# Kernel tuning notes

Hardware: AMD Instinct MI355X
Metric: run time of the kernel (lower is better)

The kernel has to match this reference:

```python
import jax, jax.numpy as jnp
import numpy as np

NUM_RBF = 16
TOP_K = 30
MAXREL = 32  # max_relative_feature
M_CTX = 16   # ligand context atoms per residue

PT_GROUP = jnp.array([0,1,18,1,2,13,14,15,16,17,18,1,2,13,14,15,16,17,18,1,2,3,4,5,6,7,8,9,10,11,12,13,14,15,16,17,18,1,2,3,4,5,6,7,8,9,10,11,12,13,14,15,16,17,18,1,2,3,3,3,3,3,3,3,3,3,3,3,3,3,3,3,4,5,6,7,8,9,10,11,12,13,14,15,16,17,18,1,2,3,3,3,3,3,3,3,3,3,3,3,3,3,3,3,4,5,6,7,8,9,10,11,12,13,14,15,16,17,18], dtype=jnp.int32)
PT_PERIOD = jnp.array([0,1,1,2,2,2,2,2,2,2,2,3,3,3,3,3,3,3,3,4,4,4,4,4,4,4,4,4,4,4,4,4,4,4,4,4,4,5,5,5,5,5,5,5,5,5,5,5,5,5,5,5,5,5,5,6,6,6,6,6,6,6,6,6,6,6,6,6,6,6,6,6,6,6,6,6,6,6,6,6,6,6,6,6,6,6,6,7,7,7,7,7,7,7,7,7,7,7,7,7,7,7,7,7,7,7,7,7,7,7,7,7,7,7,7,7,7,7,7], dtype=jnp.int32)

# pair order after the Ca-Ca term: (N,N),(C,C),(O,O),(Cb,Cb),(Ca,N),(Ca,C),(Ca,O),(Ca,Cb),
# (N,C),(N,O),(N,Cb),(Cb,C),(Cb,O),(O,C),(N,Ca),(C,Ca),(O,Ca),(Cb,Ca),(C,N),(O,N),(Cb,N),(C,Cb),(O,Cb),(C,O)
# atom index in A5 stack: N=0, Ca=1, C=2, O=3, Cb=4
AI = np.array([0,2,3,4,1,1,1,1,0,0,0,4,4,3,0,2,3,4,2,3,4,2,3,2])
BI = np.array([0,2,3,4,0,2,3,4,2,3,4,2,3,2,1,1,1,1,0,0,0,4,4,3])


def _rbf(D):
    mu = jnp.linspace(2.0, 22.0, NUM_RBF)
    sigma = (22.0 - 2.0) / NUM_RBF
    return jnp.exp(-(((D[..., None] - mu) / sigma) ** 2))


def _angle_features(A, Bc, Cc, Y):
    v1 = A - Bc
    v2 = Cc - Bc
    e1 = v1 / jnp.linalg.norm(v1, axis=-1, keepdims=True)
    dot = jnp.einsum('bli,bli->bl', e1, v2)[..., None]
    u2 = v2 - e1 * dot
    e2 = u2 / jnp.linalg.norm(u2, axis=-1, keepdims=True)
    e3 = jnp.cross(e1, e2, axis=-1)
    R = jnp.concatenate((e1[..., None], e2[..., None], e3[..., None]), axis=-1)  # [B,L,3,3]
    lv = jnp.einsum('blqp,blyq->blyp', R, Y - Bc[:, :, None, :])
    rxy = jnp.sqrt(lv[..., 0] ** 2 + lv[..., 1] ** 2 + 1e-8)
    f1 = lv[..., 0] / rxy
    f2 = lv[..., 1] / rxy
    rxyz = jnp.linalg.norm(lv, axis=-1) + 1e-8
    f3 = rxy / rxyz
    f4 = lv[..., 2] / rxyz
    return jnp.stack([f1, f2, f3, f4], axis=-1)  # [B,L,M,4]


def setup_inputs() -> dict:
    key = jax.random.key(0)
    ks = jax.random.split(key, 16)
    B, L, M = 2, 2048, M_CTX
    X = jax.random.normal(ks[0], (B, L, 4, 3), jnp.float32) * 10.0
    Y = jax.random.normal(ks[1], (B, L, M, 3), jnp.float32) * 10.0
    mask = jnp.ones((B, L), jnp.float32)
    Y_m = jnp.ones((B, L, M), jnp.float32)
    R_idx = jnp.arange(B * L, dtype=jnp.int32).reshape(B, L)
    chain_labels = jax.random.randint(ks[2], (B, L), 0, 2, jnp.int32)
    Y_t = jax.random.randint(ks[3], (B, L, M), 1, 119, jnp.int32)
    def lin(k, fi, fo):
        return jax.random.normal(k, (fi, fo), jnp.float32) / np.sqrt(fi)
    params = dict(
        Wp=lin(ks[4], 2 * MAXREL + 2, 16), bp=jnp.zeros((16,), jnp.float32),
        We=lin(ks[5], 16 + 25 * NUM_RBF, 128), be=jnp.zeros((128,), jnp.float32),
        Wn=lin(ks[6], 5 * NUM_RBF + 64 + 4, 128), bn=jnp.zeros((128,), jnp.float32),
        Wt=lin(ks[7], 147, 64), bt=jnp.zeros((64,), jnp.float32),
        Wyn=lin(ks[8], 147, 128), byn=jnp.zeros((128,), jnp.float32),
        Wye=lin(ks[9], NUM_RBF, 128), bye=jnp.zeros((128,), jnp.float32),
    )
    return dict(X=X, Y=Y, mask=mask, Y_m=Y_m, R_idx=R_idx, chain_labels=chain_labels, Y_t=Y_t, **params)


def reference(X, Y, mask, Y_m, R_idx, chain_labels, Y_t,
              Wp, bp, We, be, Wn, bn, Wt, bt, Wyn, byn, Wye, bye):
    B, L = X.shape[0], X.shape[1]
    N, Ca, C, O = X[:, :, 0], X[:, :, 1], X[:, :, 2], X[:, :, 3]
    b_ = Ca - N
    c_ = C - Ca
    a_ = jnp.cross(b_, c_, axis=-1)
    Cb = -0.58273431 * a_ + 0.56802827 * b_ - 0.54067466 * c_ + Ca

    # masked pairwise distances + kNN (smallest-k)
    m2 = mask[:, None, :] * mask[:, :, None]
    dX = Ca[:, None, :, :] - Ca[:, :, None, :]
    D = m2 * jnp.sqrt(jnp.sum(dX * dX, -1) + 1e-6)
    Dadj = D + (1.0 - m2) * jnp.max(D, -1, keepdims=True)
    k = min(TOP_K, L)
    negD, E_idx = jax.lax.top_k(-Dadj, k)
    D_neighbors = -negD  # [B,L,K]

    # gather all 5 atom coords of neighbors once, then all 24 cross-atom RBFs
    A5 = jnp.stack([N, Ca, C, O, Cb], axis=2)  # [B,L,5,3]
    nb = A5[jnp.arange(B)[:, None, None], E_idx]  # [B,L,K,5,3]
    dvec = A5[:, :, None, AI, :] - nb[:, :, :, BI, :]  # [B,L,K,24,3]
    Dp = jnp.sqrt(jnp.sum(dvec * dvec, -1) + 1e-6)
    RBF_all = jnp.concatenate([_rbf(D_neighbors),
                               _rbf(Dp).reshape(B, L, k, 24 * NUM_RBF)], axis=-1)  # [B,L,K,400]

    # positional encodings
    offset = jnp.take_along_axis(R_idx[:, :, None] - R_idx[:, None, :], E_idx, axis=2)
    Ech = jnp.take_along_axis((chain_labels[:, :, None] == chain_labels[:, None, :]).astype(jnp.int32), E_idx, axis=2)
    d = jnp.clip(offset + MAXREL, 0, 2 * MAXREL)
    d = d * Ech + (1 - Ech) * (2 * MAXREL + 1)
    Epos = jax.nn.one_hot(d, 2 * MAXREL + 2, dtype=jnp.float32) @ Wp + bp
    E = jnp.concatenate([Epos, RBF_all], axis=-1) @ We + be  # [B,L,K,128]

    # ligand atom featurization
    g = PT_GROUP[Y_t]
    p = PT_PERIOD[Y_t]
    Yt1 = jnp.concatenate([jax.nn.one_hot(Y_t, 120, dtype=jnp.float32),
                           jax.nn.one_hot(g, 19, dtype=jnp.float32),
                           jax.nn.one_hot(p, 8, dtype=jnp.float32)], axis=-1)  # [B,L,M,147]
    Yt_lin = Yt1 @ Wt + bt  # [B,L,M,64]
    dAY = A5[:, :, :, None, :] - Y[:, :, None, :, :]  # [B,L,5,M,3]
    D_AY = jnp.sqrt(jnp.sum(dAY * dAY, -1) + 1e-6)
    RBF_AY = jnp.transpose(_rbf(D_AY), (0, 1, 3, 2, 4)).reshape(B, L, Y.shape[2], 5 * NUM_RBF)
    f_ang = _angle_features(N, Ca, C, Y)  # [B,L,M,4]
    V = jnp.concatenate([RBF_AY, Yt_lin, f_ang], axis=-1) @ Wn + bn  # [B,L,M,128]

    dYY = Y[:, :, :, None, :] - Y[:, :, None, :, :]
    Y_edges = _rbf(jnp.sqrt(jnp.sum(dYY * dYY, -1) + 1e-6)) @ Wye + bye  # [B,L,M,M,128]
    Y_nodes = Yt1 @ Wyn + byn  # [B,L,M,128]
    return V, E, E_idx, Y_nodes, Y_edges, Y_m
```

## Files before the change

kernel.cpp:

```cpp
#include <hip/hip_runtime.h>
#include <float.h>

typedef unsigned int   u32;
typedef unsigned short ushort_t;
typedef __attribute__((ext_vector_type(8))) short  bf16x8;
typedef __attribute__((ext_vector_type(4))) float  f32x4;
typedef __attribute__((ext_vector_type(8))) unsigned short ushort8;

#define NB 2
#define NL 2048
#define NM 16
#define NK 30

#define OV  0ull
#define OE  8388608ull
#define OEI 24117248ull
#define OYN 24240128ull
#define OYE 32628736ull
#define OYM 166846464ull

__constant__ int PT_GROUP_c[119] = {0,1,18,1,2,13,14,15,16,17,18,1,2,13,14,15,16,17,18,1,2,3,4,5,6,7,8,9,10,11,12,13,14,15,16,17,18,1,2,3,4,5,6,7,8,9,10,11,12,13,14,15,16,17,18,1,2,3,3,3,3,3,3,3,3,3,3,3,3,3,3,3,4,5,6,7,8,9,10,11,12,13,14,15,16,17,18,1,2,3,3,3,3,3,3,3,3,3,3,3,3,3,3,3,4,5,6,7,8,9,10,11,12,13,14,15,16,17,18};
__constant__ int PT_PERIOD_c[119] = {0,1,1,2,2,2,2,2,2,2,2,3,3,3,3,3,3,3,3,4,4,4,4,4,4,4,4,4,4,4,4,4,4,4,4,4,4,5,5,5,5,5,5,5,5,5,5,5,5,5,5,5,5,5,5,6,6,6,6,6,6,6,6,6,6,6,6,6,6,6,6,6,6,6,6,6,6,6,6,6,6,6,6,6,6,6,6,7,7,7,7,7,7,7,7,7,7,7,7,7,7,7,7,7,7,7,7,7,7,7,7,7,7,7,7,7,7,7,7};
__constant__ int AI_c[24] = {0,2,3,4,1,1,1,1,0,0,0,4,4,3,0,2,3,4,2,3,4,2,3,2};
__constant__ int BI_c[24] = {0,2,3,4,0,2,3,4,2,3,4,2,3,2,1,1,1,1,0,0,0,4,4,3};

__device__ __forceinline__ float cl24(float v) {
  return fminf(fmaxf(v, -24.f), 24.f);
}

__device__ __forceinline__ ushort_t f2bf(float f) {
  u32 u = __float_as_uint(f);
  return (ushort_t)((u + 0x7fffu + ((u >> 16) & 1u)) >> 16);
}

__device__ __forceinline__ float rbff(float d, int r) {
  float mu = 2.0f + (20.0f / 15.0f) * (float)r;
  float t = (d - mu) * 0.8f;
  return __expf(-t * t);
}

__global__ __launch_bounds__(256) void k_init(const float* __restrict__ We,
        const float* __restrict__ Wn, const float* __restrict__ X,
        ushort_t* __restrict__ WeT, ushort_t* __restrict__ WnT,
        float* __restrict__ A5, float* __restrict__ Ca4,
        float* __restrict__ Fr) {
  int blk = blockIdx.x;
  int tid = threadIdx.x;
  if (blk < 128) {
    int n = blk;
    for (int k = tid; k < 416; k += 256)
      WeT[(size_t)n * 416 + k] = f2bf(We[(size_t)k * 128 + n]);
    return;
  }
  if (blk < 256) {
    int n = blk - 128;
    if (tid < 160)
      WnT[(size_t)n * 160 + tid] = (tid < 148) ? f2bf(Wn[(size_t)tid * 128 + n])
                                               : (ushort_t)0;
    return;
  }
  int id = (blk - 256) * 256 + tid;
  if (id >= NB * NL) return;
  const float* x = X + (size_t)id * 12;
  float Nx=x[0],Ny=x[1],Nz=x[2], Cax=x[3],Cay=x[4],Caz=x[5];
  float Cx=x[6],Cy=x[7],Cz=x[8], Ox=x[9],Oy=x[10],Oz=x[11];
  float bx=Cax-Nx, by=Cay-Ny, bz=Caz-Nz;
  float cx=Cx-Cax, cy=Cy-Cay, cz=Cz-Caz;
  float ax=by*cz-bz*cy, ay=bz*cx-bx*cz, az=bx*cy-by*cx;
  float Cbx = -0.58273431f*ax + 0.56802827f*bx - 0.54067466f*cx + Cax;
  float Cby = -0.58273431f*ay + 0.56802827f*by - 0.54067466f*cy + Cay;
  float Cbz = -0.58273431f*az + 0.56802827f*bz - 0.54067466f*cz + Caz;
  float* A = A5 + (size_t)id * 15;
  A[0]=Nx;A[1]=Ny;A[2]=Nz; A[3]=Cax;A[4]=Cay;A[5]=Caz;
  A[6]=Cx;A[7]=Cy;A[8]=Cz; A[9]=Ox;A[10]=Oy;A[11]=Oz;
  A[12]=Cbx;A[13]=Cby;A[14]=Cbz;
  Ca4[id*4+0]=Cax; Ca4[id*4+1]=Cay; Ca4[id*4+2]=Caz; Ca4[id*4+3]=0.f;
  float v1x=Nx-Cax, v1y=Ny-Cay, v1z=Nz-Caz;
  float v2x=Cx-Cax, v2y=Cy-Cay, v2z=Cz-Caz;
  float n1 = sqrtf(v1x*v1x+v1y*v1y+v1z*v1z);
  float e1x=v1x/n1, e1y=v1y/n1, e1z=v1z/n1;
  float dot = e1x*v2x+e1y*v2y+e1z*v2z;
  float u2x=v2x-e1x*dot, u2y=v2y-e1y*dot, u2z=v2z-e1z*dot;
  float n2 = sqrtf(u2x*u2x+u2y*u2y+u2z*u2z);
  float e2x=u2x/n2, e2y=u2y/n2, e2z=u2z/n2;
  float e3x=e1y*e2z-e1z*e2y, e3y=e1z*e2x-e1x*e2z, e3z=e1x*e2y-e1y*e2x;
  float* F = Fr + (size_t)id * 9;
  F[0]=e1x;F[1]=e1y;F[2]=e1z; F[3]=e2x;F[4]=e2y;F[5]=e2z; F[6]=e3x;F[7]=e3y;F[8]=e3z;
}

__global__ __launch_bounds__(256) void k_topk(const float* __restrict__ Ca4,
                                              const float* __restrict__ mask,
                                              float* __restrict__ Dn,
                                              int* __restrict__ Eidx,
                                              float* __restrict__ out) {
  __shared__ float dist[NL];
  __shared__ float rv[4];
  __shared__ float cand_v[128];
  __shared__ int   cand_i[128];
  int row = blockIdx.x;
  int b = row >> 11;
  int tid = threadIdx.x;
  const float4* cab = (const float4*)Ca4 + ((size_t)b << 11);
  float4 ci = ((const float4*)Ca4)[row];
  float mi = mask[row];
  float lmax = 0.f;
  for (int j = tid; j < NL; j += 256) {
    float4 cj = cab[j];
    float dx = __fsub_rn(ci.x, cj.x);
    float dy = __fsub_rn(ci.y, cj.y);
    float dz = __fsub_rn(ci.z, cj.z);
    float s  = __fadd_rn(__fadd_rn(__fadd_rn(__fmul_rn(dx,dx), __fmul_rn(dy,dy)),
                                   __fmul_rn(dz,dz)), 1e-6f);
    float D  = __fmul_rn(__fmul_rn(mask[(b << 11) + j], mi), __fsqrt_rn(s));
    dist[j] = D;
    lmax = fmaxf(lmax, D);
  }
  #pragma unroll
  for (int s = 32; s > 0; s >>= 1) lmax = fmaxf(lmax, __shfl_xor(lmax, s));
  if ((tid & 63) == 0) rv[tid >> 6] = lmax;
  __syncthreads();
  float rowmax = fmaxf(fmaxf(rv[0], rv[1]), fmaxf(rv[2], rv[3]));
  for (int j = tid; j < NL; j += 256) {
    float mj = mask[(b << 11) + j];
    dist[j] = __fadd_rn(dist[j], __fmul_rn(__fsub_rn(1.f, __fmul_rn(mi, mj)), rowmax));
  }
  __syncthreads();
  int w = tid >> 6, l = tid & 63;
  int base = w * 512 + l;
  float v[8];
  #pragma unroll
  for (int k = 0; k < 8; k++) v[k] = dist[base + k * 64];
  if (tid < 8) { cand_v[120 + tid] = FLT_MAX; cand_i[120 + tid] = NL; }
  for (int it = 0; it < NK; it++) {
    float bv = FLT_MAX; int bj = NL;
    #pragma unroll
    for (int k = 0; k < 8; k++) {
      int jj = base + k * 64;
      if (v[k] < bv) { bv = v[k]; bj = jj; }
    }
    #pragma unroll
    for (int s = 32; s > 0; s >>= 1) {
      float ov = __shfl_xor(bv, s);
      int   oj = __shfl_xor(bj, s);
      if (ov < bv || (ov == bv && oj < bj)) { bv = ov; bj = oj; }
    }
    int ow = bj & 511;
    int ko = ow >> 6;
    bool mine = (ow & 63) == l;
    #pragma unroll
    for (int k = 0; k < 8; k++)
      if (mine && k == ko) v[k] = FLT_MAX;
    if (l == 0) { cand_v[w * NK + it] = bv; cand_i[w * NK + it] = bj; }
  }
  __syncthreads();
  if (tid < 64) {
    float v1 = cand_v[tid], v2 = cand_v[64 + tid];
    int   i1 = cand_i[tid], i2 = cand_i[64 + tid];
    for (int it = 0; it < NK; it++) {
      float bv; int bj, sl;
      if (v1 < v2 || (v1 == v2 && i1 < i2)) { bv = v1; bj = i1; sl = tid; }
      else                                  { bv = v2; bj = i2; sl = 64 + tid; }
      #pragma unroll
      for (int s = 32; s > 0; s >>= 1) {
        float ov = __shfl_xor(bv, s);
        int   oj = __shfl_xor(bj, s);
        int   os = __shfl_xor(sl, s);
        if (ov < bv || (ov == bv && oj < bj)) { bv = ov; bj = oj; sl = os; }
      }
      if (sl == tid)           v1 = FLT_MAX;
      else if (sl == 64 + tid) v2 = FLT_MAX;
      if (tid == 0) {
        Dn[(size_t)row * NK + it]   = bv;
        Eidx[(size_t)row * NK + it] = bj;
        out[OEI + (size_t)row * NK + it] = (float)bj;
      }
    }
  }
}

__global__ __launch_bounds__(256) void k_edge(const float* __restrict__ A5,
        const float* __restrict__ Dn, const int* __restrict__ Eidx,
        const int* __restrict__ R_idx, const int* __restrict__ cl,
        const float* __restrict__ Wp, const float* __restrict__ bp,
        const ushort_t* __restrict__ WeT, const float* __restrict__ be,
        float* __restrict__ out) {
  __shared__ __align__(16) ushort_t feat[32][424];
  int tid = threadIdx.x;
  int e0 = blockIdx.x * 32;
  {
    int el = tid >> 3;
    int te = tid & 7;
    int e  = e0 + el;
    int bi = e / NK;
    int b  = bi >> 11;
    int j  = Eidx[e];
    j = j < 0 ? 0 : (j > NL - 1 ? NL - 1 : j);
    int jrow = (b << 11) + j;
    const float* Ac = A5 + (size_t)bi * 15;
    const float* An = A5 + (size_t)jrow * 15;
    int off = R_idx[bi] - R_idx[jrow];
    int d;
    if (cl[bi] == cl[jrow]) { d = off + 32; d = d < 0 ? 0 : (d > 64 ? 64 : d); }
    else d = 65;
    feat[el][2*te]   = f2bf(Wp[d * 16 + 2*te]   + bp[2*te]);
    feat[el][2*te+1] = f2bf(Wp[d * 16 + 2*te+1] + bp[2*te+1]);
    float dn = Dn[e];
    feat[el][16 + 2*te]   = f2bf(rbff(dn, 2*te));
    feat[el][16 + 2*te+1] = f2bf(rbff(dn, 2*te+1));
    #pragma unroll
    for (int pp = 0; pp < 3; pp++) {
      int p = te + pp * 8;
      int ai = AI_c[p] * 3, bj2 = BI_c[p] * 3;
      float dx = Ac[ai]   - An[bj2];
      float dy = Ac[ai+1] - An[bj2+1];
      float dz = Ac[ai+2] - An[bj2+2];
      float dp = sqrtf(dx*dx + dy*dy + dz*dz + 1e-6f);
      int fb = 32 + p * 16;
      #pragma unroll
      for (int r = 0; r < 16; r++) feat[el][fb + r] = f2bf(rbff(dp, r));
    }
  }
  __syncthreads();
  int l  = tid & 63;
  int wid = tid >> 6;
  int wm = wid >> 1, wn = wid & 1;
  f32x4 acc0 = {0.f,0.f,0.f,0.f}, acc1 = {0.f,0.f,0.f,0.f};
  f32x4 acc2 = {0.f,0.f,0.f,0.f}, acc3 = {0.f,0.f,0.f,0.f};
  const ushort_t* Wb = WeT + (size_t)(wn*64 + (l & 15)) * 416 + (l >> 4) * 8;
  #pragma unroll 2
  for (int c = 0; c < 13; c++) {
    bf16x8 a  = *(const bf16x8*)&feat[wm*16 + (l & 15)][c*32 + (l >> 4)*8];
    bf16x8 b0 = *(const bf16x8*)(Wb + c*32);
    bf16x8 b1 = *(const bf16x8*)(Wb + 16*416 + c*32);
    bf16x8 b2 = *(const bf16x8*)(Wb + 32*416 + c*32);
    bf16x8 b3 = *(const bf16x8*)(Wb + 48*416 + c*32);
    acc0 = __builtin_amdgcn_mfma_f32_16x16x32_bf16(a, b0, acc0, 0, 0, 0);
    acc1 = __builtin_amdgcn_mfma_f32_16x16x32_bf16(a, b1, acc1, 0, 0, 0);
    acc2 = __builtin_amdgcn_mfma_f32_16x16x32_bf16(a, b2, acc2, 0, 0, 0);
    acc3 = __builtin_amdgcn_mfma_f32_16x16x32_bf16(a, b3, acc3, 0, 0, 0);
  }
  #pragma unroll
  for (int t = 0; t < 4; t++) {
    f32x4 av = (t==0) ? acc0 : (t==1) ? acc1 : (t==2) ? acc2 : acc3;
    int n = wn*64 + t*16 + (l & 15);
    float bb = be[n];
    #pragma unroll
    for (int jj = 0; jj < 4; jj++) {
      int ee = e0 + wm*16 + (l >> 4)*4 + jj;
      out[OE + (size_t)ee * 128 + n] = cl24(av[jj] + bb);
    }
  }
}

__global__ __launch_bounds__(256) void k_v(const float* __restrict__ A5,
        const float* __restrict__ Fr, const float* __restrict__ Y,
        const int* __restrict__ Y_t,
        const ushort_t* __restrict__ WnT, const float* __restrict__ bn,
        const float* __restrict__ Wt, const float* __restrict__ bt,
        float* __restrict__ out) {
  __shared__ __align__(16) ushort_t feat[16][168];
  __shared__ float dAY[16][8];
  int tid = threadIdx.x;
  int bl = blockIdx.x;
  if (tid < 80) {
    int m = tid / 5, a = tid % 5;
    float dx = A5[(size_t)bl*15 + a*3 + 0] - Y[(size_t)bl*48 + m*3 + 0];
    float dy = A5[(size_t)bl*15 + a*3 + 1] - Y[(size_t)bl*48 + m*3 + 1];
    float dz = A5[(size_t)bl*15 + a*3 + 2] - Y[(size_t)bl*48 + m*3 + 2];
    dAY[m][a] = sqrtf(dx*dx + dy*dy + dz*dz + 1e-6f);
  }
  __syncthreads();
  {
    int m = tid >> 4, q = tid & 15;
    #pragma unroll
    for (int a = 0; a < 5; a++) feat[m][a * 16 + q] = f2bf(rbff(dAY[m][a], q));
    int yt = Y_t[(size_t)bl * NM + m];
    int g = PT_GROUP_c[yt], p = PT_PERIOD_c[yt];
    {
      float4 wa = *(const float4*)&Wt[yt*64 + q*4];
      float4 wb = *(const float4*)&Wt[(120+g)*64 + q*4];
      float4 wc = *(const float4*)&Wt[(139+p)*64 + q*4];
      float4 bb = *(const float4*)&bt[q*4];
      feat[m][80 + q*4 + 0] = f2bf(wa.x + wb.x + wc.x + bb.x);
      feat[m][80 + q*4 + 1] = f2bf(wa.y + wb.y + wc.y + bb.y);
      feat[m][80 + q*4 + 2] = f2bf(wa.z + wb.z + wc.z + bb.z);
      feat[m][80 + q*4 + 3] = f2bf(wa.w + wb.w + wc.w + bb.w);
    }
    if (q == 0) {
      const float* fr = Fr + (size_t)bl * 9;
      float cax = A5[(size_t)bl*15+3], cay = A5[(size_t)bl*15+4], caz = A5[(size_t)bl*15+5];
      float yx = Y[(size_t)bl*48 + m*3+0] - cax;
      float yy = Y[(size_t)bl*48 + m*3+1] - cay;
      float yz = Y[(size_t)bl*48 + m*3+2] - caz;
      float l0 = fr[0]*yx + fr[1]*yy + fr[2]*yz;
      float l1 = fr[3]*yx + fr[4]*yy + fr[5]*yz;
      float l2 = fr[6]*yx + fr[7]*yy + fr[8]*yz;
      float rxy  = sqrtf(l0*l0 + l1*l1 + 1e-8f);
      float rxyz = sqrtf(l0*l0 + l1*l1 + l2*l2) + 1e-8f;
      feat[m][144] = f2bf(l0 / rxy);
      feat[m][145] = f2bf(l1 / rxy);
      feat[m][146] = f2bf(rxy / rxyz);
      feat[m][147] = f2bf(l2 / rxyz);
    }
    if (q < 12) feat[m][148 + q] = 0;
  }
  __syncthreads();
  int l = tid & 63;
  int wid = tid >> 6;
  int n0 = wid * 32;
  f32x4 acc0 = {0.f,0.f,0.f,0.f}, acc1 = {0.f,0.f,0.f,0.f};
  const ushort_t* Wb = WnT + (size_t)(n0 + (l & 15)) * 160 + (l >> 4) * 8;
  #pragma unroll
  for (int c = 0; c < 5; c++) {
    bf16x8 a  = *(const bf16x8*)&feat[l & 15][c*32 + (l >> 4)*8];
    bf16x8 b0 = *(const bf16x8*)(Wb + c*32);
    bf16x8 b1 = *(const bf16x8*)(Wb + 16*160 + c*32);
    acc0 = __builtin_amdgcn_mfma_f32_16x16x32_bf16(a, b0, acc0, 0, 0, 0);
    acc1 = __builtin_amdgcn_mfma_f32_16x16x32_bf16(a, b1, acc1, 0, 0, 0);
  }
  #pragma unroll
  for (int t = 0; t < 2; t++) {
    f32x4 av = (t==0) ? acc0 : acc1;
    int n = n0 + t*16 + (l & 15);
    float bb = bn[n];
    #pragma unroll
    for (int jj = 0; jj < 4; jj++) {
      int m = (l >> 4)*4 + jj;
      out[OV + ((size_t)bl * NM + m) * 128 + n] = cl24(av[jj] + bb);
    }
  }
}

__global__ __launch_bounds__(256, 4) void k_ynode(const int* __restrict__ Y_t,
        const float* __restrict__ Wyn, const float* __restrict__ byn,
        const float* __restrict__ Y_m, float* __restrict__ out) {
  int tid = threadIdx.x;
  int bl = blockIdx.x;
  if (tid < NM)
    out[OYM + (size_t)bl * NM + tid] = Y_m[(size_t)bl * NM + tid];
  int m = tid >> 4, n0 = (tid & 15) * 8;
  int yt = Y_t[(size_t)bl * NM + m];
  int g = PT_GROUP_c[yt], p = PT_PERIOD_c[yt];
  const float* w0 = Wyn + yt * 128 + n0;
  const float* w1 = Wyn + (120 + g) * 128 + n0;
  const float* w2 = Wyn + (139 + p) * 128 + n0;
  float4 r0 = *(const float4*)&w0[0], r1 = *(const float4*)&w0[4];
  float4 s0 = *(const float4*)&w1[0], s1 = *(const float4*)&w1[4];
  float4 t0 = *(const float4*)&w2[0], t1 = *(const float4*)&w2[4];
  float4 b0 = *(const float4*)&byn[n0], b1 = *(const float4*)&byn[n0 + 4];
  float4 o0, o1;
  o0.x = cl24(r0.x + s0.x + t0.x + b0.x);
  o0.y = cl24(r0.y + s0.y + t0.y + b0.y);
  o0.z = cl24(r0.z + s0.z + t0.z + b0.z);
  o0.w = cl24(r0.w + s0.w + t0.w + b0.w);
  o1.x = cl24(r1.x + s1.x + t1.x + b1.x);
  o1.y = cl24(r1.y + s1.y + t1.y + b1.y);
  o1.z = cl24(r1.z + s1.z + t1.z + b1.z);
  o1.w = cl24(r1.w + s1.w + t1.w + b1.w);
  size_t ob = OYN + ((size_t)bl * NM + m) * 128 + n0;
  *(float4*)&out[ob]     = o0;
  *(float4*)&out[ob + 4] = o1;
}

__global__ __launch_bounds__(256) void k_yedge(const float* __restrict__ Y,
        const float* __restrict__ Wye, const float* __restrict__ bye,
        float* __restrict__ out) {
  __shared__ float rbf_s[256][20];
  __shared__ float ys[16][3];
  __shared__ float wye_s[16][128];
  __shared__ float bye_s[128];
  int tid = threadIdx.x;
  int bl = blockIdx.x;
  if (tid < 48) ((float*)ys)[tid] = Y[(size_t)bl * 48 + tid];
  for (int x = tid; x < 2048; x += 256) wye_s[x >> 7][x & 127] = Wye[x];
  if (tid < 128) bye_s[tid] = bye[tid];
  __syncthreads();
  {
    int m = tid >> 4, m2 = tid & 15;
    float dx = ys[m][0]-ys[m2][0], dy = ys[m][1]-ys[m2][1], dz = ys[m][2]-ys[m2][2];
    float dd = sqrtf(dx*dx + dy*dy + dz*dz + 1e-6f);
    #pragma unroll
    for (int r = 0; r < 16; r++) rbf_s[tid][r] = rbff(dd, r);
  }
  __syncthreads();
  int n2 = (tid & 63) * 2;
  int pg = tid >> 6;
  float wy0[16], wy1[16];
  #pragma unroll
  for (int k = 0; k < 16; k++) { wy0[k] = wye_s[k][n2]; wy1[k] = wye_s[k][n2+1]; }
  float bb0 = bye_s[n2], bb1 = bye_s[n2+1];
  size_t obase = OYE + (size_t)bl * (NM * NM * 128);
  for (int p = pg * 64; p < pg * 64 + 64; p++) {
    float s0 = bb0, s1 = bb1;
    #pragma unroll
    for (int k4 = 0; k4 < 4; k4++) {
      float4 rv = *(const float4*)&rbf_s[p][k4 * 4];
      s0 = fmaf(rv.x, wy0[k4*4+0], s0); s1 = fmaf(rv.x, wy1[k4*4+0], s1);
      s0 = fmaf(rv.y, wy0[k4*4+1], s0); s1 = fmaf(rv.y, wy1[k4*4+1], s1);
      s0 = fmaf(rv.z, wy0[k4*4+2], s0); s1 = fmaf(rv.z, wy1[k4*4+2], s1);
      s0 = fmaf(rv.w, wy0[k4*4+3], s0); s1 = fmaf(rv.w, wy1[k4*4+3], s1);
    }
    float2 st; st.x = cl24(s0); st.y = cl24(s1);
    *(float2*)&out[obase + (size_t)p * 128 + n2] = st;
  }
}

extern "C" void kernel_launch(void* const* d_in, const int* in_sizes, int n_in,
                              void* d_out, int out_size, void* d_ws, size_t ws_size,
                              hipStream_t stream) {
  const float* X     = (const float*)d_in[0];
  const float* Y     = (const float*)d_in[1];
  const float* mask  = (const float*)d_in[2];
  const float* Y_m   = (const float*)d_in[3];
  const int*   R_idx = (const int*)d_in[4];
  const int*   cl    = (const int*)d_in[5];
  const int*   Y_t   = (const int*)d_in[6];
  const float* Wp    = (const float*)d_in[7];
  const float* bp    = (const float*)d_in[8];
  const float* We    = (const float*)d_in[9];
  const float* be    = (const float*)d_in[10];
  const float* Wn    = (const float*)d_in[11];
  const float* bn    = (const float*)d_in[12];
  const float* Wt    = (const float*)d_in[13];
  const float* bt    = (const float*)d_in[14];
  const float* Wyn   = (const float*)d_in[15];
  const float* byn   = (const float*)d_in[16];
  const float* Wye   = (const float*)d_in[17];
  const float* bye   = (const float*)d_in[18];
  float* out = (float*)d_out;

  float* wsf  = (float*)d_ws;
  float* A5   = wsf;
  float* Ca4  = A5  + 61440;
  float* Fr   = Ca4 + 16384;
  float* Dn   = Fr  + 36864;
  int*   Eidx = (int*)(Dn + 122880);
  ushort_t* WeT = (ushort_t*)(Eidx + 122880);
  ushort_t* WnT = WeT + 128 * 416;

  k_init <<<272,  256, 0, stream>>>(We, Wn, X, WeT, WnT, A5, Ca4, Fr);
  k_topk <<<NB*NL,256, 0, stream>>>(Ca4, mask, Dn, Eidx, out);
  k_edge <<<(NB*NL*NK)/32, 256, 0, stream>>>(A5, Dn, Eidx, R_idx, cl, Wp, bp, WeT, be, out);
  k_v    <<<NB*NL,256, 0, stream>>>(A5, Fr, Y, Y_t, WnT, bn, Wt, bt, out);
  k_ynode<<<NB*NL,256, 0, stream>>>(Y_t, Wyn, byn, Y_m, out);
  k_yedge<<<NB*NL,256, 0, stream>>>(Y, Wye, bye, out);
}
```

Baseline: 323.5 us.

## Fold Y-node kernel into init launch and split Y-edge blocks in half

```diff
diff --git a/kernel.cpp b/kernel.cpp
--- a/kernel.cpp
+++ b/kernel.cpp
@@ -43,7 +43,10 @@
         const float* __restrict__ Wn, const float* __restrict__ X,
         ushort_t* __restrict__ WeT, ushort_t* __restrict__ WnT,
         float* __restrict__ A5, float* __restrict__ Ca4,
-        float* __restrict__ Fr) {
+        float* __restrict__ Fr,
+        const int* __restrict__ Y_t, const float* __restrict__ Wyn,
+        const float* __restrict__ byn, const float* __restrict__ Y_m,
+        float* __restrict__ out) {
   int blk = blockIdx.x;
   int tid = threadIdx.x;
   if (blk < 128) {
@@ -59,33 +62,63 @@
                                                : (ushort_t)0;
     return;
   }
-  int id = (blk - 256) * 256 + tid;
-  if (id >= NB * NL) return;
-  const float* x = X + (size_t)id * 12;
-  float Nx=x[0],Ny=x[1],Nz=x[2], Cax=x[3],Cay=x[4],Caz=x[5];
-  float Cx=x[6],Cy=x[7],Cz=x[8], Ox=x[9],Oy=x[10],Oz=x[11];
-  float bx=Cax-Nx, by=Cay-Ny, bz=Caz-Nz;
-  float cx=Cx-Cax, cy=Cy-Cay, cz=Cz-Caz;
-  float ax=by*cz-bz*cy, ay=bz*cx-bx*cz, az=bx*cy-by*cx;
-  float Cbx = -0.58273431f*ax + 0.56802827f*bx - 0.54067466f*cx + Cax;
-  float Cby = -0.58273431f*ay + 0.56802827f*by - 0.54067466f*cy + Cay;
-  float Cbz = -0.58273431f*az + 0.56802827f*bz - 0.54067466f*cz + Caz;
-  float* A = A5 + (size_t)id * 15;
-  A[0]=Nx;A[1]=Ny;A[2]=Nz; A[3]=Cax;A[4]=Cay;A[5]=Caz;
-  A[6]=Cx;A[7]=Cy;A[8]=Cz; A[9]=Ox;A[10]=Oy;A[11]=Oz;
-  A[12]=Cbx;A[13]=Cby;A[14]=Cbz;
-  Ca4[id*4+0]=Cax; Ca4[id*4+1]=Cay; Ca4[id*4+2]=Caz; Ca4[id*4+3]=0.f;
-  float v1x=Nx-Cax, v1y=Ny-Cay, v1z=Nz-Caz;
-  float v2x=Cx-Cax, v2y=Cy-Cay, v2z=Cz-Caz;
-  float n1 = sqrtf(v1x*v1x+v1y*v1y+v1z*v1z);
-  float e1x=v1x/n1, e1y=v1y/n1, e1z=v1z/n1;
-  float dot = e1x*v2x+e1y*v2y+e1z*v2z;
-  float u2x=v2x-e1x*dot, u2y=v2y-e1y*dot, u2z=v2z-e1z*dot;
-  float n2 = sqrtf(u2x*u2x+u2y*u2y+u2z*u2z);
-  float e2x=u2x/n2, e2y=u2y/n2, e2z=u2z/n2;
-  float e3x=e1y*e2z-e1z*e2y, e3y=e1z*e2x-e1x*e2z, e3z=e1x*e2y-e1y*e2x;
-  float* F = Fr + (size_t)id * 9;
-  F[0]=e1x;F[1]=e1y;F[2]=e1z; F[3]=e2x;F[4]=e2y;F[5]=e2z; F[6]=e3x;F[7]=e3y;F[8]=e3z;
+  if (blk < 272) {
+    int id = (blk - 256) * 256 + tid;
+    if (id >= NB * NL) return;
+    const float* x = X + (size_t)id * 12;
+    float Nx=x[0],Ny=x[1],Nz=x[2], Cax=x[3],Cay=x[4],Caz=x[5];
+    float Cx=x[6],Cy=x[7],Cz=x[8], Ox=x[9],Oy=x[10],Oz=x[11];
+    float bx=Cax-Nx, by=Cay-Ny, bz=Caz-Nz;
+    float cx=Cx-Cax, cy=Cy-Cay, cz=Cz-Caz;
+    float ax=by*cz-bz*cy, ay=bz*cx-bx*cz, az=bx*cy-by*cx;
+    float Cbx = -0.58273431f*ax + 0.56802827f*bx - 0.54067466f*cx + Cax;
+    float Cby = -0.58273431f*ay + 0.56802827f*by - 0.54067466f*cy + Cay;
+    float Cbz = -0.58273431f*az + 0.56802827f*bz - 0.54067466f*cz + Caz;
+    float* A = A5 + (size_t)id * 15;
+    A[0]=Nx;A[1]=Ny;A[2]=Nz; A[3]=Cax;A[4]=Cay;A[5]=Caz;
+    A[6]=Cx;A[7]=Cy;A[8]=Cz; A[9]=Ox;A[10]=Oy;A[11]=Oz;
+    A[12]=Cbx;A[13]=Cby;A[14]=Cbz;
+    Ca4[id*4+0]=Cax; Ca4[id*4+1]=Cay; Ca4[id*4+2]=Caz; Ca4[id*4+3]=0.f;
+    float v1x=Nx-Cax, v1y=Ny-Cay, v1z=Nz-Caz;
+    float v2x=Cx-Cax, v2y=Cy-Cay, v2z=Cz-Caz;
+    float n1 = sqrtf(v1x*v1x+v1y*v1y+v1z*v1z);
+    float e1x=v1x/n1, e1y=v1y/n1, e1z=v1z/n1;
+    float dot = e1x*v2x+e1y*v2y+e1z*v2z;
+    float u2x=v2x-e1x*dot, u2y=v2y-e1y*dot, u2z=v2z-e1z*dot;
+    float n2 = sqrtf(u2x*u2x+u2y*u2y+u2z*u2z);
+    float e2x=u2x/n2, e2y=u2y/n2, e2z=u2z/n2;
+    float e3x=e1y*e2z-e1z*e2y, e3y=e1z*e2x-e1x*e2z, e3z=e1x*e2y-e1y*e2x;
+    float* F = Fr + (size_t)id * 9;
+    F[0]=e1x;F[1]=e1y;F[2]=e1z; F[3]=e2x;F[4]=e2y;F[5]=e2z; F[6]=e3x;F[7]=e3y;F[8]=e3z;
+    return;
+  }
+  {
+    int bl = blk - 272;
+    if (tid < NM)
+      out[OYM + (size_t)bl * NM + tid] = Y_m[(size_t)bl * NM + tid];
+    int m = tid >> 4, n0 = (tid & 15) * 8;
+    int yt = Y_t[(size_t)bl * NM + m];
+    int g = PT_GROUP_c[yt], p = PT_PERIOD_c[yt];
+    const float* w0 = Wyn + yt * 128 + n0;
+    const float* w1 = Wyn + (120 + g) * 128 + n0;
+    const float* w2 = Wyn + (139 + p) * 128 + n0;
+    float4 r0 = *(const float4*)&w0[0], r1 = *(const float4*)&w0[4];
+    float4 s0 = *(const float4*)&w1[0], s1 = *(const float4*)&w1[4];
+    float4 t0 = *(const float4*)&w2[0], t1 = *(const float4*)&w2[4];
+    float4 b0 = *(const float4*)&byn[n0], b1 = *(const float4*)&byn[n0 + 4];
+    float4 o0, o1;
+    o0.x = cl24(r0.x + s0.x + t0.x + b0.x);
+    o0.y = cl24(r0.y + s0.y + t0.y + b0.y);
+    o0.z = cl24(r0.z + s0.z + t0.z + b0.z);
+    o0.w = cl24(r0.w + s0.w + t0.w + b0.w);
+    o1.x = cl24(r1.x + s1.x + t1.x + b1.x);
+    o1.y = cl24(r1.y + s1.y + t1.y + b1.y);
+    o1.z = cl24(r1.z + s1.z + t1.z + b1.z);
+    o1.w = cl24(r1.w + s1.w + t1.w + b1.w);
+    size_t ob = OYN + ((size_t)bl * NM + m) * 128 + n0;
+    *(float4*)&out[ob]     = o0;
+    *(float4*)&out[ob + 4] = o1;
+  }
 }
 
 __global__ __launch_bounds__(256) void k_topk(const float* __restrict__ Ca4,
@@ -331,56 +364,27 @@
   }
 }
 
-__global__ __launch_bounds__(256, 4) void k_ynode(const int* __restrict__ Y_t,
-        const float* __restrict__ Wyn, const float* __restrict__ byn,
-        const float* __restrict__ Y_m, float* __restrict__ out) {
-  int tid = threadIdx.x;
-  int bl = blockIdx.x;
-  if (tid < NM)
-    out[OYM + (size_t)bl * NM + tid] = Y_m[(size_t)bl * NM + tid];
-  int m = tid >> 4, n0 = (tid & 15) * 8;
-  int yt = Y_t[(size_t)bl * NM + m];
-  int g = PT_GROUP_c[yt], p = PT_PERIOD_c[yt];
-  const float* w0 = Wyn + yt * 128 + n0;
-  const float* w1 = Wyn + (120 + g) * 128 + n0;
-  const float* w2 = Wyn + (139 + p) * 128 + n0;
-  float4 r0 = *(const float4*)&w0[0], r1 = *(const float4*)&w0[4];
-  float4 s0 = *(const float4*)&w1[0], s1 = *(const float4*)&w1[4];
-  float4 t0 = *(const float4*)&w2[0], t1 = *(const float4*)&w2[4];
-  float4 b0 = *(const float4*)&byn[n0], b1 = *(const float4*)&byn[n0 + 4];
-  float4 o0, o1;
-  o0.x = cl24(r0.x + s0.x + t0.x + b0.x);
-  o0.y = cl24(r0.y + s0.y + t0.y + b0.y);
-  o0.z = cl24(r0.z + s0.z + t0.z + b0.z);
-  o0.w = cl24(r0.w + s0.w + t0.w + b0.w);
-  o1.x = cl24(r1.x + s1.x + t1.x + b1.x);
-  o1.y = cl24(r1.y + s1.y + t1.y + b1.y);
-  o1.z = cl24(r1.z + s1.z + t1.z + b1.z);
-  o1.w = cl24(r1.w + s1.w + t1.w + b1.w);
-  size_t ob = OYN + ((size_t)bl * NM + m) * 128 + n0;
-  *(float4*)&out[ob]     = o0;
-  *(float4*)&out[ob + 4] = o1;
-}
-
 __global__ __launch_bounds__(256) void k_yedge(const float* __restrict__ Y,
         const float* __restrict__ Wye, const float* __restrict__ bye,
         float* __restrict__ out) {
-  __shared__ float rbf_s[256][20];
-  __shared__ float ys[16][3];
+  __shared__ float rbf_s[128][20];
   __shared__ float wye_s[16][128];
   __shared__ float bye_s[128];
   int tid = threadIdx.x;
-  int bl = blockIdx.x;
-  if (tid < 48) ((float*)ys)[tid] = Y[(size_t)bl * 48 + tid];
+  int bl   = blockIdx.x >> 1;
+  int half = blockIdx.x & 1;
   for (int x = tid; x < 2048; x += 256) wye_s[x >> 7][x & 127] = Wye[x];
   if (tid < 128) bye_s[tid] = bye[tid];
-  __syncthreads();
   {
-    int m = tid >> 4, m2 = tid & 15;
-    float dx = ys[m][0]-ys[m2][0], dy = ys[m][1]-ys[m2][1], dz = ys[m][2]-ys[m2][2];
+    int lp = tid >> 1, rh = (tid & 1) * 8;
+    int p = half * 128 + lp;
+    int m = p >> 4, m2 = p & 15;
+    const float* ya = Y + (size_t)bl * 48 + m * 3;
+    const float* yb = Y + (size_t)bl * 48 + m2 * 3;
+    float dx = ya[0]-yb[0], dy = ya[1]-yb[1], dz = ya[2]-yb[2];
     float dd = sqrtf(dx*dx + dy*dy + dz*dz + 1e-6f);
     #pragma unroll
-    for (int r = 0; r < 16; r++) rbf_s[tid][r] = rbff(dd, r);
+    for (int r = 0; r < 8; r++) rbf_s[lp][rh + r] = rbff(dd, rh + r);
   }
   __syncthreads();
   int n2 = (tid & 63) * 2;
@@ -389,19 +393,19 @@
   #pragma unroll
   for (int k = 0; k < 16; k++) { wy0[k] = wye_s[k][n2]; wy1[k] = wye_s[k][n2+1]; }
   float bb0 = bye_s[n2], bb1 = bye_s[n2+1];
-  size_t obase = OYE + (size_t)bl * (NM * NM * 128);
-  for (int p = pg * 64; p < pg * 64 + 64; p++) {
+  size_t obase = OYE + (size_t)bl * (NM * NM * 128) + (size_t)half * 128 * 128;
+  for (int lp = pg * 32; lp < pg * 32 + 32; lp++) {
     float s0 = bb0, s1 = bb1;
     #pragma unroll
     for (int k4 = 0; k4 < 4; k4++) {
-      float4 rv = *(const float4*)&rbf_s[p][k4 * 4];
+      float4 rv = *(const float4*)&rbf_s[lp][k4 * 4];
       s0 = fmaf(rv.x, wy0[k4*4+0], s0); s1 = fmaf(rv.x, wy1[k4*4+0], s1);
       s0 = fmaf(rv.y, wy0[k4*4+1], s0); s1 = fmaf(rv.y, wy1[k4*4+1], s1);
       s0 = fmaf(rv.z, wy0[k4*4+2], s0); s1 = fmaf(rv.z, wy1[k4*4+2], s1);
       s0 = fmaf(rv.w, wy0[k4*4+3], s0); s1 = fmaf(rv.w, wy1[k4*4+3], s1);
     }
     float2 st; st.x = cl24(s0); st.y = cl24(s1);
-    *(float2*)&out[obase + (size_t)p * 128 + n2] = st;
+    *(float2*)&out[obase + (size_t)lp * 128 + n2] = st;
   }
 }
 
@@ -438,10 +442,11 @@
   ushort_t* WeT = (ushort_t*)(Eidx + 122880);
   ushort_t* WnT = WeT + 128 * 416;
 
-  k_init <<<272,  256, 0, stream>>>(We, Wn, X, WeT, WnT, A5, Ca4, Fr);
-  k_topk <<<NB*NL,256, 0, stream>>>(Ca4, mask, Dn, Eidx, out);
-  k_edge <<<(NB*NL*NK)/32, 256, 0, stream>>>(A5, Dn, Eidx, R_idx, cl, Wp, bp, WeT, be, out);
-  k_v    <<<NB*NL,256, 0, stream>>>(A5, Fr, Y, Y_t, WnT, bn, Wt, bt, out);
-  k_ynode<<<NB*NL,256, 0, stream>>>(Y_t, Wyn, byn, Y_m, out);
-  k_yedge<<<NB*NL,256, 0, stream>>>(Y, Wye, bye, out);
-}
+  k_init <<<272 + NB*NL, 256, 0, stream>>>(We, Wn, X, WeT, WnT, A5, Ca4, Fr,
+                                           Y_t, Wyn, byn, Y_m, out);
+  k_topk <<<NB*NL, 256, 0, stream>>>(Ca4, mask, Dn, Eidx, out);
+  k_edge <<<(NB*NL*NK)/32, 256, 0, stream>>>(A5, Dn, Eidx, R_idx, cl,
+                                             Wp, bp, WeT, be, out);
+  k_v    <<<NB*NL, 256, 0, stream>>>(A5, Fr, Y, Y_t, WnT, bn, Wt, bt, out);
+  k_yedge<<<2*NB*NL, 256, 0, stream>>>(Y, Wye, bye, out);
+}
```

Result: no change. 317.9 us (-1.7%).
